# Kernel tuning notes

Measured on AMD Instinct MI355X. Metric: run time of the kernel, lower is better.

The kernel has to match this reference:

```python
import jax, jax.numpy as jnp
import numpy as np

DIM, NH, HD = 1536, 12, 128
C = HD // 2            # 64 complex (half) dims per head
BANDS = (C - 2 * (C // 3), C // 3, C // 3)   # (22, 21, 21) for T/H/W
EPS = 1e-6
F, Hg, Wg = 6, 20, 32
S = F * Hg * Wg
MAX_LEN = 1024


def _rope_tables(max_len=MAX_LEN):
    # Wan-style 1D rope params per band, concatenated along channel dim -> [max_len, 64]
    pos = np.arange(max_len, dtype=np.float64)
    cos_l, sin_l = [], []
    for bd in BANDS:
        inv = 1.0 / (10000.0 ** (np.arange(bd, dtype=np.float64) / bd))
        ang = np.outer(pos, inv)
        cos_l.append(np.cos(ang))
        sin_l.append(np.sin(ang))
    return (np.concatenate(cos_l, 1).astype(np.float32),
            np.concatenate(sin_l, 1).astype(np.float32))


def setup_inputs() -> dict:
    key = jax.random.key(0)
    ks = jax.random.split(key, 8)
    std = 0.02
    fc, fs = _rope_tables()
    return {
        "x": jax.random.normal(ks[0], (1, S, DIM), jnp.float32),
        "Wq": jax.random.normal(ks[1], (DIM, DIM), jnp.float32) * std,
        "bq": jnp.zeros((DIM,), jnp.float32),
        "Wk": jax.random.normal(ks[2], (DIM, DIM), jnp.float32) * std,
        "bk": jnp.zeros((DIM,), jnp.float32),
        "Wv": jax.random.normal(ks[3], (DIM, DIM), jnp.float32) * std,
        "bv": jnp.zeros((DIM,), jnp.float32),
        "Wo": jax.random.normal(ks[4], (DIM, DIM), jnp.float32) * std,
        "bo": jnp.zeros((DIM,), jnp.float32),
        "gq": jnp.ones((DIM,), jnp.float32),
        "gk": jnp.ones((DIM,), jnp.float32),
        "freqs_cos": jnp.asarray(fc),
        "freqs_sin": jnp.asarray(fs),
        "f": F, "h": Hg, "w": Wg,
    }


def _rmsnorm(t, g):
    t = t.astype(jnp.float32)
    return t * jax.lax.rsqrt(jnp.mean(t * t, axis=-1, keepdims=True) + EPS) * g


def _grid_freqs(tab, f, h, w):
    # tab: [max_len, 64] -> [f*h*w, 64] via T/H/W band broadcast (mirrors torch expand+cat)
    o1, o2 = BANDS[0], BANDS[0] + BANDS[1]
    t = jnp.broadcast_to(tab[:f, None, None, :o1], (f, h, w, BANDS[0]))
    hh = jnp.broadcast_to(tab[None, :h, None, o1:o2], (f, h, w, BANDS[1]))
    ww = jnp.broadcast_to(tab[None, None, :w, o2:C], (f, h, w, BANDS[2]))
    return jnp.concatenate([t, hh, ww], axis=-1).reshape(f * h * w, 1, C)


def _rope_apply(t, fc, fs):
    # t: [B, S, n, d]; complex mul (a+ib)*(cos+isin) on pairs of channels
    B, Sl, n, d = t.shape
    tr = t.astype(jnp.float32).reshape(B, Sl, n, C, 2)
    a, b = tr[..., 0], tr[..., 1]
    fc = fc[None]  # [1, S, 1, C]
    fs = fs[None]
    out_r = a * fc - b * fs
    out_i = a * fs + b * fc
    return jnp.stack([out_r, out_i], axis=-1).reshape(B, Sl, n, d)


def reference(x, Wq, bq, Wk, bk, Wv, bv, Wo, bo, gq, gk, freqs_cos, freqs_sin, f, h, w):
    B, Sl, _ = x.shape
    q = _rmsnorm(x @ Wq.T + bq, gq).reshape(B, Sl, NH, HD)
    k = _rmsnorm(x @ Wk.T + bk, gk).reshape(B, Sl, NH, HD)
    v = (x @ Wv.T + bv).reshape(B, Sl, NH, HD)

    fc = _grid_freqs(freqs_cos, f, h, w)
    fs = _grid_freqs(freqs_sin, f, h, w)
    q = _rope_apply(q, fc, fs)
    k = _rope_apply(k, fc, fs)

    scale = 1.0 / jnp.sqrt(jnp.float32(HD))
    scores = jnp.einsum('bqnd,bknd->bnqk', q, k) * scale
    p = jax.nn.softmax(scores, axis=-1)
    o = jnp.einsum('bnqk,bknd->bqnd', p, v.astype(jnp.float32))
    o = o.reshape(B, Sl, DIM)
    return o @ Wo.T + bo
```

## Files before the change

kernel.cpp:

```cpp
#include <hip/hip_runtime.h>
#include <hip/hip_bf16.h>
#include <cstdint>

#define DIM 1536
#define NHEADS 12
#define HD 128
#define SEQ 3840
#define SCL2F 0.1275365308119098f
#define THRRAW 90.50966799187809f

typedef float f32x4 __attribute__((ext_vector_type(4)));
typedef __bf16 bf16x8 __attribute__((ext_vector_type(8)));
typedef __bf16 bf16x4 __attribute__((ext_vector_type(4)));
typedef __bf16 bf16x2 __attribute__((ext_vector_type(2)));
typedef unsigned int u32;
typedef u32 u32x4 __attribute__((ext_vector_type(4)));

#define GLLD(g, l) __builtin_amdgcn_global_load_lds( \
    (const __attribute__((address_space(1))) void*)(g), \
    (__attribute__((address_space(3))) void*)(l), 16, 0, 0)

__global__ __launch_bounds__(256) void cvt_bf16_5(
    const float* __restrict__ s0, const float* __restrict__ s1, const float* __restrict__ s2,
    const float* __restrict__ s3, const float* __restrict__ s4,
    __bf16* __restrict__ d0, __bf16* __restrict__ d1, __bf16* __restrict__ d2,
    __bf16* __restrict__ d3, __bf16* __restrict__ d4,
    int n4_0, int n4_w) {
    const float* src; __bf16* dst; int n4;
    switch (blockIdx.y) {
        case 0: src = s0; dst = d0; n4 = n4_0; break;
        case 1: src = s1; dst = d1; n4 = n4_w; break;
        case 2: src = s2; dst = d2; n4 = n4_w; break;
        case 3: src = s3; dst = d3; n4 = n4_w; break;
        default: src = s4; dst = d4; n4 = n4_w; break;
    }
    int i = blockIdx.x * 256 + threadIdx.x;
    if (i < n4) {
        f32x4 v = ((const f32x4*)src)[i];
        bf16x4 o;
        o[0] = (__bf16)v[0]; o[1] = (__bf16)v[1];
        o[2] = (__bf16)v[2]; o[3] = (__bf16)v[3];
        ((bf16x4*)dst)[i] = o;
    }
}

template <int OUTF32>
__global__ __launch_bounds__(256, 2) void gemm256(
    const __bf16* __restrict__ A,
    const __bf16* __restrict__ B0, const __bf16* __restrict__ B1, const __bf16* __restrict__ B2,
    const float* __restrict__ bias0, const float* __restrict__ bias1, const float* __restrict__ bias2,
    void* __restrict__ C0v, void* __restrict__ C1v, void* __restrict__ C2v,
    int N, int K) {
    const int orig = blockIdx.x;
    const int nwg = gridDim.x;
    const int qq_ = nwg >> 3, rr_ = nwg & 7;
    const int xcd = orig & 7, off = orig >> 3;
    const int wgid = (xcd < rr_ ? xcd * (qq_ + 1) : rr_ * (qq_ + 1) + (xcd - rr_) * qq_) + off;
    const int z = wgid / 180;
    const int rem = wgid - z * 180;
    const int by = rem / 12;
    const int bx = rem - by * 12;

    const __bf16* B = B0; const float* bias = bias0; void* Cv = C0v;
    if (z == 1) { B = B1; bias = bias1; Cv = C1v; }
    else if (z == 2) { B = B2; bias = bias2; Cv = C2v; }

    __shared__ __bf16 sA[3][256 * 32];
    __shared__ __bf16 sB[3][128 * 32];

    const int t = threadIdx.x;
    const int wid = t >> 6, lane = t & 63;
    const int lr = lane & 15, lg = lane >> 4;
    const int wr = (wid >> 1) * 128, wc = (wid & 1) * 64;

    const __bf16* pa = A + ((long long)by * 256 + (t >> 2)) * K + (t & 3) * 8;
    const __bf16* pb = B + ((long long)bx * 128 + (t >> 2)) * K + (t & 3) * 8;
    const int ldsbase = wid * 512;

    auto stage = [&](int kk, int bufi) {
#pragma unroll
        for (int r = 0; r < 4; r++)
            GLLD(pa + (long long)(r * 64) * K + kk, &sA[bufi][r * 2048 + ldsbase]);
#pragma unroll
        for (int r = 0; r < 2; r++)
            GLLD(pb + (long long)(r * 64) * K + kk, &sB[bufi][r * 2048 + ldsbase]);
    };

    f32x4 acc[8][4] = {};
    const int NT = K / 32;

    stage(0, 0);
    stage(32, 1);
    asm volatile("s_waitcnt vmcnt(6)" ::: "memory");
    __builtin_amdgcn_s_barrier();
    __builtin_amdgcn_sched_barrier(0);

    int c0 = 0, c2 = 2;
#pragma unroll 1
    for (int i = 0; i < NT; i++) {
        const __bf16* sAc = &sA[0][0] + c0 * (256 * 32);
        const __bf16* sBc = &sB[0][0] + c0 * (128 * 32);
        bf16x8 af[8], bfr[4];
#pragma unroll
        for (int mI = 0; mI < 8; mI++)
            af[mI] = *(const bf16x8*)(sAc + (wr + mI * 16 + lr) * 32 + lg * 8);
#pragma unroll
        for (int nI = 0; nI < 4; nI++)
            bfr[nI] = *(const bf16x8*)(sBc + (wc + nI * 16 + lr) * 32 + lg * 8);
        if (i + 2 < NT) stage((i + 2) * 32, c2);

        __builtin_amdgcn_s_setprio(1);
#pragma unroll
        for (int mI = 0; mI < 8; mI++) {
            acc[mI][0] = __builtin_amdgcn_mfma_f32_16x16x32_bf16(af[mI], bfr[0], acc[mI][0], 0, 0, 0);
            acc[mI][1] = __builtin_amdgcn_mfma_f32_16x16x32_bf16(af[mI], bfr[1], acc[mI][1], 0, 0, 0);
        }
        __builtin_amdgcn_s_setprio(0);
        __builtin_amdgcn_s_barrier();
        __builtin_amdgcn_s_setprio(1);
#pragma unroll
        for (int mI = 0; mI < 8; mI++) {
            acc[mI][2] = __builtin_amdgcn_mfma_f32_16x16x32_bf16(af[mI], bfr[2], acc[mI][2], 0, 0, 0);
            acc[mI][3] = __builtin_amdgcn_mfma_f32_16x16x32_bf16(af[mI], bfr[3], acc[mI][3], 0, 0, 0);
        }
        __builtin_amdgcn_s_setprio(0);

        if (i + 2 < NT) asm volatile("s_waitcnt vmcnt(6)" ::: "memory");
        else            asm volatile("s_waitcnt vmcnt(0)" ::: "memory");
        __builtin_amdgcn_s_barrier();
        __builtin_amdgcn_sched_barrier(0);
        c0 = (c0 == 2) ? 0 : c0 + 1;
        c2 = (c2 == 2) ? 0 : c2 + 1;
    }

    const int cb = bx * 128 + wc;
    const int rb_ = by * 256 + wr;
#pragma unroll
    for (int nI = 0; nI < 4; nI++) {
        int col = cb + nI * 16 + lr;
        float bv = bias[col];
#pragma unroll
        for (int mI = 0; mI < 8; mI++) {
            int row0 = rb_ + mI * 16 + lg * 4;
#pragma unroll
            for (int r = 0; r < 4; r++) {
                float v = acc[mI][nI][r] + bv;
                if (OUTF32) ((float*)Cv)[(long long)(row0 + r) * N + col] = v;
                else ((__bf16*)Cv)[(long long)(row0 + r) * N + col] = (__bf16)v;
            }
        }
    }
}

__global__ __launch_bounds__(256) void norm_tr(
    const __bf16* __restrict__ qpre, const __bf16* __restrict__ kpre,
    const float* __restrict__ gq, const float* __restrict__ gk,
    const float* __restrict__ fcos, const float* __restrict__ fsin,
    __bf16* __restrict__ Qb, __bf16* __restrict__ Kb,
    const __bf16* __restrict__ vpre, __bf16* __restrict__ Vtb) {
    __shared__ __bf16 tile[64][68];
    __shared__ float red[4];
    const int t = threadIdx.x;

    if (blockIdx.y == 2) {
        const int bxx = blockIdx.x;
        if (bxx >= (SEQ / 64) * (DIM / 64)) return;
        const int sb = (bxx % (SEQ / 64)) * 64, cb = (bxx / (SEQ / 64)) * 64;
        const int tx = t & 15, ty = t >> 4;
#pragma unroll
        for (int i = 0; i < 4; i++) {
            int r = ty + i * 16;
            bf16x4 v = *(const bf16x4*)(vpre + (size_t)(sb + r) * DIM + cb + tx * 4);
            *(bf16x4*)&tile[r][tx * 4] = v;
        }
        __syncthreads();
        int s0 = sb + tx * 4;
        int j = (s0 >> 2) & 7;
        int u = (j < 4) ? (j << 1) : ((j << 1) - 7);
        int sp = (s0 & ~31) + (u << 2);
#pragma unroll
        for (int i = 0; i < 4; i++) {
            int c = ty + i * 16;
            bf16x4 v;
            v[0] = tile[tx * 4 + 0][c]; v[1] = tile[tx * 4 + 1][c];
            v[2] = tile[tx * 4 + 2][c]; v[3] = tile[tx * 4 + 3][c];
            *(bf16x4*)(Vtb + (size_t)(cb + c) * SEQ + sp) = v;
        }
        return;
    }

    const __bf16* pre = blockIdx.y ? kpre : qpre;
    const float* gvec = blockIdx.y ? gk : gq;
    __bf16* out = blockIdx.y ? Kb : Qb;
    const int s = blockIdx.x;
    float a[3], b[3];
    float ss = 0.f;
#pragma unroll
    for (int j = 0; j < 3; j++) {
        int p = t + 256 * j;
        bf16x2 v = *(const bf16x2*)(pre + (size_t)s * DIM + 2 * p);
        a[j] = (float)v[0]; b[j] = (float)v[1];
        ss += a[j] * a[j] + b[j] * b[j];
    }
    for (int off = 32; off; off >>= 1) ss += __shfl_down(ss, off);
    if ((t & 63) == 0) red[t >> 6] = ss;
    __syncthreads();
    float mean = (red[0] + red[1] + red[2] + red[3]) * (1.f / DIM);
    float rms = rsqrtf(mean + 1e-6f);
    const int fi = s / 640, hi2 = (s % 640) >> 5, wi = s & 31;
#pragma unroll
    for (int j = 0; j < 3; j++) {
        int p = t + 256 * j;
        int c = p & 63;
        int pos = (c < 22) ? fi : ((c < 43) ? hi2 : wi);
        float fc = fcos[pos * 64 + c];
        float fs = fsin[pos * 64 + c];
        float av = a[j] * rms * gvec[2 * p];
        float bv = b[j] * rms * gvec[2 * p + 1];
        float orr = av * fc - bv * fs;
        float oi = av * fs + bv * fc;
        int hh = p >> 6;
        bf16x2 o; o[0] = (__bf16)orr; o[1] = (__bf16)oi;
        *(bf16x2*)(out + ((size_t)hh * SEQ + s) * HD + 2 * c) = o;
    }
}

__global__ __launch_bounds__(256, 3) void attn_split(
    const __bf16* __restrict__ Q, const __bf16* __restrict__ Kk,
    const __bf16* __restrict__ Vp,
    float* __restrict__ pacc,
    float2* __restrict__ pml) {
    __shared__ __bf16 Ks[2][32 * 128];
    __shared__ __bf16 Vs[2][128 * 32];
    const int bid = blockIdx.x;
    const int task = (bid & 7) * 90 + (bid >> 3);
    const int half = task & 1;
    const int hq = task >> 1;
    const int h = hq / 30;
    const int qb = hq % 30;
    const int t = threadIdx.x;
    const int wv = t >> 6;
    const int lane = t & 63;
    const int lq = lane & 15, g = lane >> 4;
    const int q0 = qb * 128 + wv * 32;
    const int kvbase = half * (SEQ / 2);
    const __bf16* Qh = Q + (size_t)h * SEQ * HD;
    const __bf16* Kh = Kk + (size_t)h * SEQ * HD;
    const __bf16* Vh = Vp + (size_t)h * HD * SEQ;

    bf16x8 qf[2][4];
#pragma unroll
    for (int qg = 0; qg < 2; qg++)
#pragma unroll
        for (int c = 0; c < 4; c++)
            qf[qg][c] = *(const bf16x8*)(Qh + (size_t)(q0 + qg * 16 + lq) * HD + c * 32 + g * 8);

    f32x4 acc[8][2] = {};
    float m[2] = {-1e30f, -1e30f};
    float lp[2] = {0.f, 0.f};

    const int krow0 = wv * 4 + (lane >> 4);
    const int kcb = ((lane & 15) * 16) ^ ((krow0 & 7) << 4);
    const __bf16* kp = Kh + (size_t)(kvbase + krow0) * HD + (kcb >> 1);
    const __bf16* vp = Vh + (size_t)(wv * 16 + (lane >> 2)) * SEQ + kvbase + (lane & 3) * 8;
    auto stage = [&](int i, int b) {
        const __bf16* kpi = kp + (size_t)i * 32 * HD;
        const __bf16* vpi = vp + i * 32;
        GLLD(kpi,           &Ks[b][wv * 512]);
        GLLD(kpi + 16 * HD, &Ks[b][(wv + 4) * 512]);
        GLLD(vpi,            &Vs[b][wv * 512]);
        GLLD(vpi + 64 * SEQ, &Vs[b][(wv + 4) * 512]);
    };

    stage(0, 0);
    int buf = 0;
    const int kswz = (lq & 7) << 3;
#pragma unroll 1
    for (int i = 0; i < 60; i++) {
        __syncthreads();
        if (i + 1 < 60) stage(i + 1, buf ^ 1);
        const __bf16* Kb_ = &Ks[buf][0];
        const __bf16* Vb_ = &Vs[buf][0];

        f32x4 sc[2][2] = {};
        __builtin_amdgcn_s_setprio(1);
#pragma unroll
        for (int c = 0; c < 4; c++) {
            int cb = (c * 32 + g * 8) ^ kswz;
            bf16x8 k0 = *(const bf16x8*)(Kb_ + lq * 128 + cb);
            bf16x8 k1 = *(const bf16x8*)(Kb_ + (16 + lq) * 128 + cb);
            sc[0][0] = __builtin_amdgcn_mfma_f32_16x16x32_bf16(k0, qf[0][c], sc[0][0], 0, 0, 0);
            sc[0][1] = __builtin_amdgcn_mfma_f32_16x16x32_bf16(k0, qf[1][c], sc[0][1], 0, 0, 0);
            sc[1][0] = __builtin_amdgcn_mfma_f32_16x16x32_bf16(k1, qf[0][c], sc[1][0], 0, 0, 0);
            sc[1][1] = __builtin_amdgcn_mfma_f32_16x16x32_bf16(k1, qf[1][c], sc[1][1], 0, 0, 0);
        }
        __builtin_amdgcn_s_setprio(0);

        bf16x8 vf[8];
#pragma unroll
        for (int dt = 0; dt < 8; dt++)
            vf[dt] = *(const bf16x8*)(Vb_ + (dt * 16 + lq) * 32 + g * 8);

        bf16x8 pa[2];
#pragma unroll
        for (int qg = 0; qg < 2; qg++) {
            float pm = fmaxf(fmaxf(sc[0][qg][0], sc[0][qg][1]), sc[0][qg][2]);
            pm = fmaxf(fmaxf(pm, sc[0][qg][3]), sc[1][qg][0]);
            pm = fmaxf(fmaxf(pm, sc[1][qg][1]), sc[1][qg][2]);
            pm = fmaxf(pm, sc[1][qg][3]);
            if (!__all(pm <= m[qg] + THRRAW)) {
                pm = fmaxf(pm, __shfl_xor(pm, 16));
                pm = fmaxf(pm, __shfl_xor(pm, 32));
                float mn = fmaxf(m[qg], pm);
                float al = __builtin_amdgcn_exp2f(SCL2F * (m[qg] - mn));
                m[qg] = mn; lp[qg] *= al;
#pragma unroll
                for (int dt = 0; dt < 8; dt++)
#pragma unroll
                    for (int r = 0; r < 4; r++) acc[dt][qg][r] *= al;
            }
            float ms = SCL2F * m[qg];
            float p[8], ls = 0.f;
#pragma unroll
            for (int r = 0; r < 4; r++) { p[r] = __builtin_amdgcn_exp2f(SCL2F * sc[0][qg][r] - ms); ls += p[r]; }
#pragma unroll
            for (int r = 0; r < 4; r++) { p[4 + r] = __builtin_amdgcn_exp2f(SCL2F * sc[1][qg][r] - ms); ls += p[4 + r]; }
            lp[qg] += ls;
#pragma unroll
            for (int i2 = 0; i2 < 8; i2++) pa[qg][i2] = (__bf16)p[i2];
        }

        __builtin_amdgcn_s_setprio(1);
#pragma unroll
        for (int dt = 0; dt < 8; dt++) {
            acc[dt][0] = __builtin_amdgcn_mfma_f32_16x16x32_bf16(vf[dt], pa[0], acc[dt][0], 0, 0, 0);
            acc[dt][1] = __builtin_amdgcn_mfma_f32_16x16x32_bf16(vf[dt], pa[1], acc[dt][1], 0, 0, 0);
        }
        __builtin_amdgcn_s_setprio(0);
        buf ^= 1;
    }

#pragma unroll
    for (int qg = 0; qg < 2; qg++) {
        float lps = lp[qg];
        lps += __shfl_xor(lps, 16);
        lps += __shfl_xor(lps, 32);
        const size_t qrow = (size_t)(half * NHEADS + h) * SEQ + q0 + qg * 16 + lq;
        if (g == 0) pml[qrow] = float2{m[qg], lps};
#pragma unroll
        for (int dt = 0; dt < 8; dt++)
            *(f32x4*)(pacc + qrow * HD + dt * 16 + g * 4) = acc[dt][qg];
    }
}

__global__ __launch_bounds__(256) void attn_merge(
    const float* __restrict__ pacc, const float2* __restrict__ pml,
    __bf16* __restrict__ ob) {
    const int t = threadIdx.x;
    const int qq = blockIdx.x * 8 + (t >> 5);
    const int d = (t & 31) * 4;
    float2 a = pml[qq], b = pml[NHEADS * SEQ + qq];
    float M = fmaxf(a.x, b.x);
    float w0 = __builtin_amdgcn_exp2f(SCL2F * (a.x - M));
    float w1 = __builtin_amdgcn_exp2f(SCL2F * (b.x - M));
    float den = 1.f / (a.y * w0 + b.y * w1);
    f32x4 n0 = *(const f32x4*)(pacc + (size_t)qq * HD + d);
    f32x4 n1 = *(const f32x4*)(pacc + ((size_t)NHEADS * SEQ + qq) * HD + d);
    int h = qq / SEQ, s = qq % SEQ;
    bf16x4 o;
#pragma unroll
    for (int r = 0; r < 4; r++) o[r] = (__bf16)((n0[r] * w0 + n1[r] * w1) * den);
    *(bf16x4*)(ob + (size_t)s * DIM + h * HD + d) = o;
}

__global__ __launch_bounds__(256, 4) void attn_single(
    const __bf16* __restrict__ Q, const __bf16* __restrict__ Kk,
    const __bf16* __restrict__ Vp, __bf16* __restrict__ O) {
    __shared__ __bf16 Ks[2][32 * 128];
    __shared__ __bf16 Vs[2][128 * 32];
    const int bid = blockIdx.x;
    const int task = (bid & 7) * 90 + (bid >> 3);
    const int h = task / 60;
    const int qb = task % 60;
    const int t = threadIdx.x;
    const int wv = t >> 6;
    const int lane = t & 63;
    const int lq = lane & 15, g = lane >> 4;
    const int q0 = qb * 64 + wv * 16;
    const __bf16* Qh = Q + (size_t)h * SEQ * HD;
    const __bf16* Kh = Kk + (size_t)h * SEQ * HD;
    const __bf16* Vh = Vp + (size_t)h * HD * SEQ;
    bf16x8 qf[4];
#pragma unroll
    for (int c = 0; c < 4; c++)
        qf[c] = *(const bf16x8*)(Qh + (size_t)(q0 + lq) * HD + c * 32 + g * 8);
    f32x4 acc[8] = {};
    float m = -1e30f, lp = 0.f;
    const int krow_in = lane >> 4;
    const int vrow_in = lane >> 2;
    const int vce = (lane & 3) * 8;
    auto stage = [&](int kv0, int b) {
#pragma unroll
        for (int c = wv; c < 16; c += 4) {
            if (c < 8) {
                int r = c * 4 + krow_in;
                int cb = ((lane & 15) * 16) ^ ((r & 7) << 4);
                GLLD(Kh + (size_t)(kv0 + r) * HD + (cb >> 1), &Ks[b][c * 512]);
            } else {
                int cc = c - 8;
                int rd = cc * 16 + vrow_in;
                GLLD(Vh + (size_t)rd * SEQ + kv0 + vce, &Vs[b][cc * 512]);
            }
        }
    };
    stage(0, 0);
    int buf = 0;
    const int kswz = (lq & 7) << 3;
#pragma unroll 1
    for (int i = 0; i < 120; i++) {
        __syncthreads();
        if (i + 1 < 120) stage((i + 1) * 32, buf ^ 1);
        const __bf16* Kb_ = &Ks[buf][0];
        const __bf16* Vb_ = &Vs[buf][0];
        f32x4 sc0 = {0.f, 0.f, 0.f, 0.f}, sc1 = {0.f, 0.f, 0.f, 0.f};
#pragma unroll
        for (int c = 0; c < 4; c++) {
            int cb = (c * 32 + g * 8) ^ kswz;
            bf16x8 k0 = *(const bf16x8*)(Kb_ + lq * 128 + cb);
            bf16x8 k1 = *(const bf16x8*)(Kb_ + (16 + lq) * 128 + cb);
            sc0 = __builtin_amdgcn_mfma_f32_16x16x32_bf16(k0, qf[c], sc0, 0, 0, 0);
            sc1 = __builtin_amdgcn_mfma_f32_16x16x32_bf16(k1, qf[c], sc1, 0, 0, 0);
        }
        bf16x8 vf[8];
#pragma unroll
        for (int dt = 0; dt < 8; dt++)
            vf[dt] = *(const bf16x8*)(Vb_ + (dt * 16 + lq) * 32 + g * 8);
        float pm = fmaxf(fmaxf(sc0[0], sc0[1]), sc0[2]);
        pm = fmaxf(fmaxf(pm, sc0[3]), sc1[0]);
        pm = fmaxf(fmaxf(pm, sc1[1]), sc1[2]);
        pm = fmaxf(pm, sc1[3]);
        if (!__all(pm <= m + THRRAW)) {
            pm = fmaxf(pm, __shfl_xor(pm, 16));
            pm = fmaxf(pm, __shfl_xor(pm, 32));
            float mn = fmaxf(m, pm);
            float al = __builtin_amdgcn_exp2f(SCL2F * (m - mn));
            m = mn; lp *= al;
#pragma unroll
            for (int dt = 0; dt < 8; dt++)
#pragma unroll
                for (int r = 0; r < 4; r++) acc[dt][r] *= al;
        }
        float ms = SCL2F * m;
        float p[8], ls = 0.f;
#pragma unroll
        for (int r = 0; r < 4; r++) { p[r] = __builtin_amdgcn_exp2f(SCL2F * sc0[r] - ms); ls += p[r]; }
#pragma unroll
        for (int r = 0; r < 4; r++) { p[4 + r] = __builtin_amdgcn_exp2f(SCL2F * sc1[r] - ms); ls += p[4 + r]; }
        lp += ls;
        bf16x8 pa;
#pragma unroll
        for (int i2 = 0; i2 < 8; i2++) pa[i2] = (__bf16)p[i2];
#pragma unroll
        for (int dt = 0; dt < 8; dt++)
            acc[dt] = __builtin_amdgcn_mfma_f32_16x16x32_bf16(vf[dt], pa, acc[dt], 0, 0, 0);
        buf ^= 1;
    }
    float lps = lp;
    lps += __shfl_xor(lps, 16);
    lps += __shfl_xor(lps, 32);
    float inv = 1.f / lps;
#pragma unroll
    for (int dt = 0; dt < 8; dt++) {
        bf16x4 o;
#pragma unroll
        for (int r = 0; r < 4; r++) o[r] = (__bf16)(acc[dt][r] * inv);
        *(bf16x4*)(O + (size_t)(q0 + lq) * DIM + h * HD + dt * 16 + g * 4) = o;
    }
}

extern "C" void kernel_launch(void* const* d_in, const int* in_sizes, int n_in,
                              void* d_out, int out_size, void* d_ws, size_t ws_size,
                              hipStream_t stream) {
    const float* x = (const float*)d_in[0];
    const float* Wq = (const float*)d_in[1];
    const float* bq = (const float*)d_in[2];
    const float* Wk = (const float*)d_in[3];
    const float* bk = (const float*)d_in[4];
    const float* Wv = (const float*)d_in[5];
    const float* bv = (const float*)d_in[6];
    const float* Wo = (const float*)d_in[7];
    const float* bo = (const float*)d_in[8];
    const float* gq = (const float*)d_in[9];
    const float* gk = (const float*)d_in[10];
    const float* fcos = (const float*)d_in[11];
    const float* fsin = (const float*)d_in[12];
    float* out = (float*)d_out;

    char* p = (char*)d_ws;
    const size_t SZ_SD = (size_t)SEQ * DIM * 2;
    const size_t SZ_W = (size_t)DIM * DIM * 2;
    __bf16* xb   = (__bf16*)p;  p += SZ_SD;
    __bf16* Wob  = (__bf16*)p;  p += SZ_W;
    __bf16* Wqb  = (__bf16*)p;  p += SZ_W;
    __bf16* Wkb  = (__bf16*)p;  p += SZ_W;
    __bf16* Wvb  = (__bf16*)p;  p += SZ_W;
    __bf16* qpre = (__bf16*)p;  p += SZ_SD;
    __bf16* kpre = (__bf16*)p;  p += SZ_SD;
    __bf16* vpre = (__bf16*)p;  p += SZ_SD;
    __bf16* Kb   = (__bf16*)p;  p += SZ_SD;
    __bf16* Vtb  = (__bf16*)p;  p += SZ_SD;
    float2* pml  = (float2*)p;  p += sizeof(float2) * 2 * NHEADS * SEQ;
    float* pacc = (float*)Wqb;
    __bf16* Qb = xb;
    const bool split_ok = ws_size >= (size_t)(p - (char*)d_ws);

    const int n4_x = SEQ * DIM / 4;
    const int n4_w = DIM * DIM / 4;
    cvt_bf16_5<<<dim3((n4_x + 255) / 256, 5), 256, 0, stream>>>(
        x, Wq, Wk, Wv, Wo, xb, Wqb, Wkb, Wvb, Wob, n4_x, n4_w);

    gemm256<0><<<dim3(540), 256, 0, stream>>>(
        xb, Wqb, Wkb, Wvb, bq, bk, bv, qpre, kpre, vpre, DIM, DIM);

    norm_tr<<<dim3(SEQ, 3), 256, 0, stream>>>(
        qpre, kpre, gq, gk, fcos, fsin, Qb, Kb, vpre, Vtb);

    if (split_ok) {
        __bf16* ob = Kb;
        attn_split<<<dim3(720), 256, 0, stream>>>(Qb, Kb, Vtb, pacc, pml);
        attn_merge<<<dim3(NHEADS * SEQ / 8), 256, 0, stream>>>(pacc, pml, ob);
        gemm256<1><<<dim3(180), 256, 0, stream>>>(
            ob, Wob, Wob, Wob, bo, bo, bo, out, out, out, DIM, DIM);
    } else {
        __bf16* ob = qpre;
        attn_single<<<dim3(720), 256, 0, stream>>>(Qb, Kb, Vtb, ob);
        gemm256<1><<<dim3(180), 256, 0, stream>>>(
            ob, Wob, Wob, Wob, bo, bo, bo, out, out, out, DIM, DIM);
    }
}
```

Measured before the change: 264.6 us.

## Double KV tile to 64 rows per stage with XOR-swizzled V layout

The split attention kernel now stages 64 K/V rows per iteration instead of 32, which halves the loop trip count and the number of barriers. Each stage is consumed as two 32-row sub-steps. V tiles in LDS now use an XOR swizzle on the column offset to avoid bank conflicts with the wider 64-column rows. The cost is doubled LDS use (64KB per block) and the occupancy hint drops from 3 to 2 blocks per CU, so there is less latency hiding across waves.

After: 291.0 us. +10.0%, slower.

```diff
diff --git a/kernel.cpp b/kernel.cpp
--- a/kernel.cpp
+++ b/kernel.cpp
@@ -225,13 +225,13 @@
     }
 }
 
-__global__ __launch_bounds__(256, 3) void attn_split(
+__global__ __launch_bounds__(256, 2) void attn_split(
     const __bf16* __restrict__ Q, const __bf16* __restrict__ Kk,
     const __bf16* __restrict__ Vp,
     float* __restrict__ pacc,
     float2* __restrict__ pml) {
-    __shared__ __bf16 Ks[2][32 * 128];
-    __shared__ __bf16 Vs[2][128 * 32];
+    __shared__ __bf16 Ks[2][64 * 128];
+    __shared__ __bf16 Vs[2][128 * 64];
     const int bid = blockIdx.x;
     const int task = (bid & 7) * 90 + (bid >> 3);
     const int half = task & 1;
@@ -259,84 +259,91 @@
     float m[2] = {-1e30f, -1e30f};
     float lp[2] = {0.f, 0.f};
 
-    const int krow0 = wv * 4 + (lane >> 4);
-    const int kcb = ((lane & 15) * 16) ^ ((krow0 & 7) << 4);
-    const __bf16* kp = Kh + (size_t)(kvbase + krow0) * HD + (kcb >> 1);
-    const __bf16* vp = Vh + (size_t)(wv * 16 + (lane >> 2)) * SEQ + kvbase + (lane & 3) * 8;
-    auto stage = [&](int i, int b) {
-        const __bf16* kpi = kp + (size_t)i * 32 * HD;
-        const __bf16* vpi = vp + i * 32;
-        GLLD(kpi,           &Ks[b][wv * 512]);
-        GLLD(kpi + 16 * HD, &Ks[b][(wv + 4) * 512]);
-        GLLD(vpi,            &Vs[b][wv * 512]);
-        GLLD(vpi + 64 * SEQ, &Vs[b][(wv + 4) * 512]);
+    const int krow_in = lane >> 4;
+    const int vrow_in = lane >> 3;
+    const int vce = (((lane & 7) ^ (lane >> 3))) * 8;
+    auto stage = [&](int kv0, int b) {
+        for (int c = wv; c < 32; c += 4) {
+            if (c < 16) {
+                int r = c * 4 + krow_in;
+                int cb = ((lane & 15) * 16) ^ ((r & 7) << 4);
+                GLLD(Kh + (size_t)(kv0 + r) * HD + (cb >> 1), &Ks[b][c * 512]);
+            } else {
+                int cc = c - 16;
+                int rd = cc * 8 + vrow_in;
+                GLLD(Vh + (size_t)rd * SEQ + kv0 + vce, &Vs[b][cc * 512]);
+            }
+        }
     };
 
-    stage(0, 0);
+    stage(kvbase, 0);
     int buf = 0;
     const int kswz = (lq & 7) << 3;
 #pragma unroll 1
-    for (int i = 0; i < 60; i++) {
+    for (int i = 0; i < 30; i++) {
         __syncthreads();
-        if (i + 1 < 60) stage(i + 1, buf ^ 1);
+        if (i + 1 < 30) stage(kvbase + (i + 1) * 64, buf ^ 1);
         const __bf16* Kb_ = &Ks[buf][0];
         const __bf16* Vb_ = &Vs[buf][0];
 
-        f32x4 sc[2][2] = {};
-        __builtin_amdgcn_s_setprio(1);
-#pragma unroll
-        for (int c = 0; c < 4; c++) {
-            int cb = (c * 32 + g * 8) ^ kswz;
-            bf16x8 k0 = *(const bf16x8*)(Kb_ + lq * 128 + cb);
-            bf16x8 k1 = *(const bf16x8*)(Kb_ + (16 + lq) * 128 + cb);
-            sc[0][0] = __builtin_amdgcn_mfma_f32_16x16x32_bf16(k0, qf[0][c], sc[0][0], 0, 0, 0);
-            sc[0][1] = __builtin_amdgcn_mfma_f32_16x16x32_bf16(k0, qf[1][c], sc[0][1], 0, 0, 0);
-            sc[1][0] = __builtin_amdgcn_mfma_f32_16x16x32_bf16(k1, qf[0][c], sc[1][0], 0, 0, 0);
-            sc[1][1] = __builtin_amdgcn_mfma_f32_16x16x32_bf16(k1, qf[1][c], sc[1][1], 0, 0, 0);
-        }
-        __builtin_amdgcn_s_setprio(0);
-
-        bf16x8 vf[8];
-#pragma unroll
-        for (int dt = 0; dt < 8; dt++)
-            vf[dt] = *(const bf16x8*)(Vb_ + (dt * 16 + lq) * 32 + g * 8);
-
-        bf16x8 pa[2];
-#pragma unroll
-        for (int qg = 0; qg < 2; qg++) {
-            float pm = fmaxf(fmaxf(sc[0][qg][0], sc[0][qg][1]), sc[0][qg][2]);
-            pm = fmaxf(fmaxf(pm, sc[0][qg][3]), sc[1][qg][0]);
-            pm = fmaxf(fmaxf(pm, sc[1][qg][1]), sc[1][qg][2]);
-            pm = fmaxf(pm, sc[1][qg][3]);
-            if (!__all(pm <= m[qg] + THRRAW)) {
-                pm = fmaxf(pm, __shfl_xor(pm, 16));
-                pm = fmaxf(pm, __shfl_xor(pm, 32));
-                float mn = fmaxf(m[qg], pm);
-                float al = __builtin_amdgcn_exp2f(SCL2F * (m[qg] - mn));
-                m[qg] = mn; lp[qg] *= al;
-#pragma unroll
-                for (int dt = 0; dt < 8; dt++)
-#pragma unroll
-                    for (int r = 0; r < 4; r++) acc[dt][qg][r] *= al;
+#pragma unroll
+        for (int s = 0; s < 2; s++) {
+            f32x4 sc[2][2] = {};
+            __builtin_amdgcn_s_setprio(1);
+#pragma unroll
+            for (int c = 0; c < 4; c++) {
+                int cb = (c * 32 + g * 8) ^ kswz;
+                bf16x8 k0 = *(const bf16x8*)(Kb_ + (s * 32 + lq) * 128 + cb);
+                bf16x8 k1 = *(const bf16x8*)(Kb_ + (s * 32 + 16 + lq) * 128 + cb);
+                sc[0][0] = __builtin_amdgcn_mfma_f32_16x16x32_bf16(k0, qf[0][c], sc[0][0], 0, 0, 0);
+                sc[0][1] = __builtin_amdgcn_mfma_f32_16x16x32_bf16(k0, qf[1][c], sc[0][1], 0, 0, 0);
+                sc[1][0] = __builtin_amdgcn_mfma_f32_16x16x32_bf16(k1, qf[0][c], sc[1][0], 0, 0, 0);
+                sc[1][1] = __builtin_amdgcn_mfma_f32_16x16x32_bf16(k1, qf[1][c], sc[1][1], 0, 0, 0);
             }
-            float ms = SCL2F * m[qg];
-            float p[8], ls = 0.f;
-#pragma unroll
-            for (int r = 0; r < 4; r++) { p[r] = __builtin_amdgcn_exp2f(SCL2F * sc[0][qg][r] - ms); ls += p[r]; }
-#pragma unroll
-            for (int r = 0; r < 4; r++) { p[4 + r] = __builtin_amdgcn_exp2f(SCL2F * sc[1][qg][r] - ms); ls += p[4 + r]; }
-            lp[qg] += ls;
-#pragma unroll
-            for (int i2 = 0; i2 < 8; i2++) pa[qg][i2] = (__bf16)p[i2];
-        }
-
-        __builtin_amdgcn_s_setprio(1);
-#pragma unroll
-        for (int dt = 0; dt < 8; dt++) {
-            acc[dt][0] = __builtin_amdgcn_mfma_f32_16x16x32_bf16(vf[dt], pa[0], acc[dt][0], 0, 0, 0);
-            acc[dt][1] = __builtin_amdgcn_mfma_f32_16x16x32_bf16(vf[dt], pa[1], acc[dt][1], 0, 0, 0);
-        }
-        __builtin_amdgcn_s_setprio(0);
+            __builtin_amdgcn_s_setprio(0);
+
+            bf16x8 vf[8];
+#pragma unroll
+            for (int dt = 0; dt < 8; dt++)
+                vf[dt] = *(const bf16x8*)(Vb_ + (dt * 16 + lq) * 64 + ((s * 32 + g * 8) ^ kswz));
+
+            bf16x8 pa[2];
+#pragma unroll
+            for (int qg = 0; qg < 2; qg++) {
+                float pm = fmaxf(fmaxf(sc[0][qg][0], sc[0][qg][1]), sc[0][qg][2]);
+                pm = fmaxf(fmaxf(pm, sc[0][qg][3]), sc[1][qg][0]);
+                pm = fmaxf(fmaxf(pm, sc[1][qg][1]), sc[1][qg][2]);
+                pm = fmaxf(pm, sc[1][qg][3]);
+                if (!__all(pm <= m[qg] + THRRAW)) {
+                    pm = fmaxf(pm, __shfl_xor(pm, 16));
+                    pm = fmaxf(pm, __shfl_xor(pm, 32));
+                    float mn = fmaxf(m[qg], pm);
+                    float al = __builtin_amdgcn_exp2f(SCL2F * (m[qg] - mn));
+                    m[qg] = mn; lp[qg] *= al;
+#pragma unroll
+                    for (int dt = 0; dt < 8; dt++)
+#pragma unroll
+                        for (int r = 0; r < 4; r++) acc[dt][qg][r] *= al;
+                }
+                float ms = SCL2F * m[qg];
+                float p[8], ls = 0.f;
+#pragma unroll
+                for (int r = 0; r < 4; r++) { p[r] = __builtin_amdgcn_exp2f(SCL2F * sc[0][qg][r] - ms); ls += p[r]; }
+#pragma unroll
+                for (int r = 0; r < 4; r++) { p[4 + r] = __builtin_amdgcn_exp2f(SCL2F * sc[1][qg][r] - ms); ls += p[4 + r]; }
+                lp[qg] += ls;
+#pragma unroll
+                for (int i2 = 0; i2 < 8; i2++) pa[qg][i2] = (__bf16)p[i2];
+            }
+
+            __builtin_amdgcn_s_setprio(1);
+#pragma unroll
+            for (int dt = 0; dt < 8; dt++) {
+                acc[dt][0] = __builtin_amdgcn_mfma_f32_16x16x32_bf16(vf[dt], pa[0], acc[dt][0], 0, 0, 0);
+                acc[dt][1] = __builtin_amdgcn_mfma_f32_16x16x32_bf16(vf[dt], pa[1], acc[dt][1], 0, 0, 0);
+            }
+            __builtin_amdgcn_s_setprio(0);
+        }
         buf ^= 1;
     }
 
```
